# Kernel optimization log

Hardware: AMD Instinct MI355X
Metric: run time of the kernel (lower is better)

Reference implementation:

```python
import jax, jax.numpy as jnp
import numpy as np

NEG_INF = -1.0e12  # matches torch's -1e12 mask value
LEAKY_SLOPE = 0.01  # nn.LeakyReLU default


def setup_inputs() -> dict:
    key = jax.random.key(0)
    k1, k2, k3, k4 = jax.random.split(key, 4)
    B, N, in_c, out_c = 8, 2048, 64, 64
    inp = jax.random.normal(k1, (B, N, in_c), dtype=jnp.float32)
    adj = jax.random.randint(k2, (B, N, N), 0, 2, dtype=jnp.int32)
    W = jax.random.normal(k3, (in_c, out_c), dtype=jnp.float32) * (1.0 / np.sqrt(in_c))
    a = jax.random.normal(k4, (2 * out_c, 1), dtype=jnp.float32) * 0.1
    return {"inp": inp, "adj": adj, "W": W, "a": a}


def reference(inp, adj, W, a):
    # GAT layer. The original builds an O(B*N^2*2*out_c) concat tensor;
    # a^T [h_i || h_j] decomposes exactly into (h_i . a1) + (h_j . a2).
    out_c = W.shape[1]
    h = jnp.einsum('bni,io->bno', inp, W)          # [B,N,out_c]
    a1 = a[:out_c, 0]                               # [out_c]
    a2 = a[out_c:, 0]                               # [out_c]
    e_i = h @ a1                                    # [B,N] source term
    e_j = h @ a2                                    # [B,N] target term
    e = e_i[:, :, None] + e_j[:, None, :]           # [B,N,N]
    e = jnp.where(e > 0, e, LEAKY_SLOPE * e)        # LeakyReLU(0.01)
    masked = jnp.where(adj > 0, e, NEG_INF)
    attention = jax.nn.softmax(masked, axis=2)      # [B,N,N]
    # dropout omitted (eval mode / deterministic reference)
    h_prime = jnp.einsum('bnm,bmo->bno', attention, h)  # [B,N,out_c]
    return h_prime
```

## Files before the change

kernel.cpp:

```cpp
#include <hip/hip_runtime.h>
#include <cstdint>

#define BB 8
#define NN 2048
#define CC 64
#define TI 128
#define JSPLIT 2
#define KRANGE (NN / JSPLIT)
#define JCH 128
#define NCH (KRANGE / JCH)

typedef __attribute__((ext_vector_type(8))) _Float16 f16x8;
typedef __attribute__((ext_vector_type(4))) float f32x4;
typedef __attribute__((ext_vector_type(4))) unsigned int u32x4;
typedef __attribute__((ext_vector_type(4))) int i32x4;

static const size_t WS_H   = 0;
static const size_t WS_E1  = WS_H  + (size_t)BB*NN*CC;
static const size_t WS_E2  = WS_E1 + (size_t)BB*NN;
static const size_t WS_HT  = WS_E2 + (size_t)BB*NN;
static const size_t WS_ACC = WS_HT + (size_t)BB*CC*NN/2;
static const size_t WS_Z   = WS_ACC + (size_t)JSPLIT*BB*NN*CC;

#define GL16(g, l) __builtin_amdgcn_global_load_lds( \
    (const __attribute__((address_space(1))) void*)(g), \
    (__attribute__((address_space(3))) void*)(uint32_t)(uintptr_t)(l), 16, 0, 0)
#define GL4(g, l) __builtin_amdgcn_global_load_lds( \
    (const __attribute__((address_space(1))) void*)(g), \
    (__attribute__((address_space(3))) void*)(uint32_t)(uintptr_t)(l), 4, 0, 0)
#define WAIT0()  asm volatile("s_waitcnt vmcnt(0)" ::: "memory")
#define BAR()    __builtin_amdgcn_s_barrier()

__global__ __launch_bounds__(256) void k1_proj(const float* __restrict__ inp,
        const float* __restrict__ Wm, const float* __restrict__ av,
        float* __restrict__ h, float* __restrict__ e1, float* __restrict__ e2) {
    __shared__ float inp_lds[256];
    int t = threadIdx.x;
    size_t base = (size_t)blockIdx.x * 256;
    inp_lds[t] = inp[base + t];
    __syncthreads();
    int r = t >> 6;
    int c = t & 63;
    const float* irow = &inp_lds[r * 64];
    float acc = 0.f;
    #pragma unroll
    for (int k = 0; k < 64; k++) acc = fmaf(irow[k], Wm[k * 64 + c], acc);
    size_t row = (size_t)blockIdx.x * 4 + r;
    h[row * 64 + c] = acc;
    float v1 = acc * av[c];
    float v2 = acc * av[64 + c];
    #pragma unroll
    for (int o = 32; o > 0; o >>= 1) {
        v1 += __shfl_down(v1, o);
        v2 += __shfl_down(v2, o);
    }
    if (c == 0) { e1[row] = v1; e2[row] = v2; }
}

__global__ __launch_bounds__(256) void k1b_transpose(const float* __restrict__ h,
        unsigned short* __restrict__ hT) {
    __shared__ float tile[64][65];
    int t = threadIdx.x;
    int b = blockIdx.x >> 5;
    int i0 = (blockIdx.x & 31) * 64;
    const float* hb = h + ((size_t)b * NN + i0) * CC;
    #pragma unroll
    for (int q = 0; q < 16; q++) {
        int idx = q * 256 + t;
        tile[idx >> 6][idx & 63] = hb[idx];
    }
    __syncthreads();
    int c = t & 63;
    int rgrp = t >> 6;
    unsigned int uh[8];
    #pragma unroll
    for (int p = 0; p < 8; p++) {
        unsigned int pack_h = 0;
        #pragma unroll
        for (int s = 0; s < 2; s++) {
            float v = tile[rgrp * 16 + p * 2 + s][c];
            _Float16 fh = (_Float16)v;
            unsigned int u = (unsigned int)__builtin_bit_cast(unsigned short, fh);
            pack_h |= u << (16 * s);
        }
        uh[p] = pack_h;
    }
    size_t off = ((size_t)b * 64 + c) * NN + i0 + rgrp * 16;
    u32x4* dh = (u32x4*)(hT + off);
    dh[0] = u32x4{uh[0], uh[1], uh[2], uh[3]};
    dh[1] = u32x4{uh[4], uh[5], uh[6], uh[7]};
}

__global__ __launch_bounds__(512, 1) void k2_mfma(const int* __restrict__ adj,
        const unsigned short* __restrict__ hT,
        const float* __restrict__ e1, const float* __restrict__ e2,
        float* __restrict__ accp, float* __restrict__ zp) {
    __shared__ __align__(16) char smem[135168];
    float* e2L = (float*)(smem + 131072);

    int bid = blockIdx.x;
    int b    = bid & 7;
    int rest = bid >> 3;
    int s    = rest & 1;
    int tile = rest >> 1;
    int i0 = tile * TI;
    int jbase = s * KRANGE;

    int t = threadIdx.x;
    int w = t >> 6;
    int l = t & 63;
    int col = l & 15;
    int kg  = l >> 4;

    const int* adjrow = adj + ((size_t)b * NN + i0 + w * 16 + col) * NN + jbase;
    float e1v = e1[(size_t)b * NN + i0 + w * 16 + col];
    const float* e2b = e2 + (size_t)b * NN;
    const unsigned short* hTb = hT + (size_t)b * 64 * NN;

    f32x4 acc[4];
    #pragma unroll
    for (int n = 0; n < 4; n++) acc[n] = f32x4{0.f, 0.f, 0.f, 0.f};
    f32x4 accZ = f32x4{0.f, 0.f, 0.f, 0.f};

    _Float16 onev = (_Float16)1.0f, zerov = (_Float16)0.0f;
    f16x8 onesf;
    #pragma unroll
    for (int i = 0; i < 8; i++) onesf[i] = (col == 0) ? onev : zerov;

    i32x4 aA[8], aB[8];

#define ADJP(jcN, arr) { \
    _Pragma("unroll") \
    for (int q = 0; q < 4; q++) { \
        const i32x4* ap = (const i32x4*)(adjrow + (jcN) * JCH + q * 32 + kg * 8); \
        arr[2 * q]     = ap[0]; \
        arr[2 * q + 1] = ap[1]; \
    } \
}

#define COMPUTE(jcN, arr) { \
    _Pragma("unroll") \
    for (int ks4 = 0; ks4 < 4; ks4++) { \
        int ks = (jcN) * 4 + ks4; \
        int krel = ks * 32 + kg * 8; \
        i32x4 a0 = arr[2 * ks4]; \
        i32x4 a1 = arr[2 * ks4 + 1]; \
        f32x4 e20 = *(const f32x4*)(e2L + krel); \
        f32x4 e21 = *(const f32x4*)(e2L + krel + 4); \
        float xs[8] = {e20.x, e20.y, e20.z, e20.w, e21.x, e21.y, e21.z, e21.w}; \
        int ms[8] = {a0.x, a0.y, a0.z, a0.w, a1.x, a1.y, a1.z, a1.w}; \
        f16x8 pf; \
        _Pragma("unroll") \
        for (int i = 0; i < 8; i++) { \
            float x = e1v + xs[i]; \
            x = fmaxf(x, 0.01f * x); \
            x = __expf(x); \
            x = (ms[i] > 0) ? x : 0.0f; \
            pf[i] = (_Float16)x; \
        } \
        int g = ks * 4 + kg; \
        _Pragma("unroll") \
        for (int n = 0; n < 4; n++) { \
            int c = n * 16 + col; \
            int p = (g & 120) | ((g ^ c) & 7); \
            f16x8 hv = __builtin_bit_cast(f16x8, *(const f32x4*)(smem + c * 2048 + p * 16)); \
            acc[n] = __builtin_amdgcn_mfma_f32_16x16x32_f16(pf, hv, acc[n], 0, 0, 0); \
        } \
        accZ = __builtin_amdgcn_mfma_f32_16x16x32_f16(pf, onesf, accZ, 0, 0, 0); \
    } \
}

    ADJP(0, aA);

    #pragma unroll
    for (int it = 0; it < 16; it++) {
        int k16 = it * 8 + w;
        int c   = k16 >> 1;
        int p   = (k16 & 1) * 64 + l;
        int g   = (p & 120) | ((p ^ c) & 7);
        const unsigned short* src = hTb + (size_t)c * NN + jbase + g * 8;
        GL16(src, smem + (size_t)k16 * 1024);
    }
    #pragma unroll
    for (int it = 0; it < 2; it++) {
        GL4(e2b + jbase + it * 512 + w * 64 + l,
            smem + 131072 + (it * 512 + w * 64) * 4);
    }
    WAIT0();
    BAR();

    #pragma unroll
    for (int jc = 0; jc < NCH; jc += 2) {
        ADJP(jc + 1, aB);
        COMPUTE(jc, aA);
        if (jc + 2 < NCH) ADJP(jc + 2, aA);
        COMPUTE(jc + 1, aB);
    }

    size_t orow = (size_t)s * BB * NN + (size_t)b * NN + i0 + w * 16 + kg * 4;
    float* accout = accp + orow * CC;
    #pragma unroll
    for (int n = 0; n < 4; n++) {
        #pragma unroll
        for (int r = 0; r < 4; r++) {
            accout[(size_t)r * CC + n * 16 + col] = acc[n][r];
        }
    }
    if (col == 0) {
        #pragma unroll
        for (int r = 0; r < 4; r++) zp[orow + r] = accZ[r];
    }
#undef ADJP
#undef COMPUTE
}

__global__ __launch_bounds__(256) void k3_final(const float* __restrict__ accp,
        const float* __restrict__ zp, float* __restrict__ out) {
    int idx = blockIdx.x * 256 + threadIdx.x;
    const int TOT4 = BB * NN * CC / 4;
    if (idx >= TOT4) return;
    int row = idx >> 4;
    f32x4 s0 = ((const f32x4*)accp)[idx];
    f32x4 s1 = ((const f32x4*)accp)[idx + TOT4];
    float z = zp[row] + zp[row + BB * NN];
    float inv = (z > 0.f) ? (1.0f / z) : 0.f;
    f32x4 o;
    o.x = (s0.x + s1.x) * inv;
    o.y = (s0.y + s1.y) * inv;
    o.z = (s0.z + s1.z) * inv;
    o.w = (s0.w + s1.w) * inv;
    ((f32x4*)out)[idx] = o;
}

extern "C" void kernel_launch(void* const* d_in, const int* in_sizes, int n_in,
                              void* d_out, int out_size, void* d_ws, size_t ws_size,
                              hipStream_t stream) {
    const float* inp = (const float*)d_in[0];
    const int*   adj = (const int*)d_in[1];
    const float* Wm  = (const float*)d_in[2];
    const float* av  = (const float*)d_in[3];
    float* ws = (float*)d_ws;
    float* h    = ws + WS_H;
    float* e1   = ws + WS_E1;
    float* e2   = ws + WS_E2;
    unsigned short* hT = (unsigned short*)(ws + WS_HT);
    float* accp = ws + WS_ACC;
    float* zp   = ws + WS_Z;
    float* out  = (float*)d_out;

    k1_proj<<<BB * NN / 4, 256, 0, stream>>>(inp, Wm, av, h, e1, e2);
    k1b_transpose<<<BB * (NN / 64), 256, 0, stream>>>(h, hT);
    k2_mfma<<<BB * (NN / TI) * JSPLIT, 512, 0, stream>>>(adj, hT, e1, e2, accp, zp);
    k3_final<<<(BB * NN * CC / 4 + 255) / 256, 256, 0, stream>>>(accp, zp, out);
}
```

Before: 44.89 us.

## Fuse projection with fp16 transpose and deepen adjacency prefetch to three buffers

Merges the projection kernel and the transpose kernel into one. Each block now computes a 64-row tile of h in LDS-backed registers and writes e1/e2 plus the transposed fp16 h directly, so the fp32 h round trip and one launch go away. Separately, the main MFMA kernel now uses three adjacency register buffers instead of two, issuing loads two chunks ahead to hide more global-memory latency. The cost is more register pressure in the main kernel and a heavier, lower-parallelism projection kernel.

After: 136.4 us. 3.04x slower.

```diff
diff --git a/kernel.cpp b/kernel.cpp
--- a/kernel.cpp
+++ b/kernel.cpp
@@ -15,8 +15,7 @@
 typedef __attribute__((ext_vector_type(4))) unsigned int u32x4;
 typedef __attribute__((ext_vector_type(4))) int i32x4;
 
-static const size_t WS_H   = 0;
-static const size_t WS_E1  = WS_H  + (size_t)BB*NN*CC;
+static const size_t WS_E1  = 0;
 static const size_t WS_E2  = WS_E1 + (size_t)BB*NN;
 static const size_t WS_HT  = WS_E2 + (size_t)BB*NN;
 static const size_t WS_ACC = WS_HT + (size_t)BB*CC*NN/2;
@@ -31,61 +30,60 @@
 #define WAIT0()  asm volatile("s_waitcnt vmcnt(0)" ::: "memory")
 #define BAR()    __builtin_amdgcn_s_barrier()
 
-__global__ __launch_bounds__(256) void k1_proj(const float* __restrict__ inp,
+__global__ __launch_bounds__(256) void k1_fused(const float* __restrict__ inp,
         const float* __restrict__ Wm, const float* __restrict__ av,
-        float* __restrict__ h, float* __restrict__ e1, float* __restrict__ e2) {
-    __shared__ float inp_lds[256];
-    int t = threadIdx.x;
-    size_t base = (size_t)blockIdx.x * 256;
-    inp_lds[t] = inp[base + t];
-    __syncthreads();
-    int r = t >> 6;
-    int c = t & 63;
-    const float* irow = &inp_lds[r * 64];
-    float acc = 0.f;
-    #pragma unroll
-    for (int k = 0; k < 64; k++) acc = fmaf(irow[k], Wm[k * 64 + c], acc);
-    size_t row = (size_t)blockIdx.x * 4 + r;
-    h[row * 64 + c] = acc;
-    float v1 = acc * av[c];
-    float v2 = acc * av[64 + c];
-    #pragma unroll
-    for (int o = 32; o > 0; o >>= 1) {
-        v1 += __shfl_down(v1, o);
-        v2 += __shfl_down(v2, o);
-    }
-    if (c == 0) { e1[row] = v1; e2[row] = v2; }
-}
-
-__global__ __launch_bounds__(256) void k1b_transpose(const float* __restrict__ h,
-        unsigned short* __restrict__ hT) {
-    __shared__ float tile[64][65];
+        unsigned short* __restrict__ hT, float* __restrict__ e1, float* __restrict__ e2) {
+    __shared__ float inpL[64][65];
+    __shared__ float WL[64][65];
     int t = threadIdx.x;
     int b = blockIdx.x >> 5;
     int i0 = (blockIdx.x & 31) * 64;
-    const float* hb = h + ((size_t)b * NN + i0) * CC;
+    const float* ib = inp + ((size_t)b * NN + i0) * CC;
     #pragma unroll
     for (int q = 0; q < 16; q++) {
         int idx = q * 256 + t;
-        tile[idx >> 6][idx & 63] = hb[idx];
+        inpL[idx >> 6][idx & 63] = ib[idx];
+        WL[idx >> 6][idx & 63]   = Wm[idx];
     }
     __syncthreads();
-    int c = t & 63;
-    int rgrp = t >> 6;
+    int rg = t >> 6;
+    int c  = t & 63;
+    float a1 = av[c], a2 = av[64 + c];
+    float hv[16];
+    #pragma unroll
+    for (int p = 0; p < 16; p++) {
+        float acc = 0.f;
+        #pragma unroll
+        for (int k = 0; k < 64; k++) acc = fmaf(inpL[rg * 16 + p][k], WL[k][c], acc);
+        hv[p] = acc;
+    }
+    #pragma unroll
+    for (int p = 0; p < 16; p++) {
+        float v1 = hv[p] * a1;
+        float v2 = hv[p] * a2;
+        #pragma unroll
+        for (int o = 32; o > 0; o >>= 1) {
+            v1 += __shfl_down(v1, o);
+            v2 += __shfl_down(v2, o);
+        }
+        if (c == 0) {
+            size_t row = (size_t)b * NN + i0 + rg * 16 + p;
+            e1[row] = v1;
+            e2[row] = v2;
+        }
+    }
     unsigned int uh[8];
     #pragma unroll
-    for (int p = 0; p < 8; p++) {
-        unsigned int pack_h = 0;
-        #pragma unroll
-        for (int s = 0; s < 2; s++) {
-            float v = tile[rgrp * 16 + p * 2 + s][c];
-            _Float16 fh = (_Float16)v;
-            unsigned int u = (unsigned int)__builtin_bit_cast(unsigned short, fh);
-            pack_h |= u << (16 * s);
-        }
-        uh[p] = pack_h;
-    }
-    size_t off = ((size_t)b * 64 + c) * NN + i0 + rgrp * 16;
+    for (int p8 = 0; p8 < 8; p8++) {
+        unsigned int pack = 0;
+        #pragma unroll
+        for (int ss = 0; ss < 2; ss++) {
+            _Float16 fh = (_Float16)hv[p8 * 2 + ss];
+            pack |= ((unsigned int)__builtin_bit_cast(unsigned short, fh)) << (16 * ss);
+        }
+        uh[p8] = pack;
+    }
+    size_t off = ((size_t)b * 64 + c) * NN + i0 + rg * 16;
     u32x4* dh = (u32x4*)(hT + off);
     dh[0] = u32x4{uh[0], uh[1], uh[2], uh[3]};
     dh[1] = u32x4{uh[4], uh[5], uh[6], uh[7]};
@@ -127,7 +125,7 @@
     #pragma unroll
     for (int i = 0; i < 8; i++) onesf[i] = (col == 0) ? onev : zerov;
 
-    i32x4 aA[8], aB[8];
+    i32x4 aA[8], aB[8], aC[8];
 
 #define ADJP(jcN, arr) { \
     _Pragma("unroll") \
@@ -171,6 +169,8 @@
 }
 
     ADJP(0, aA);
+    ADJP(1, aB);
+    ADJP(2, aC);
 
     #pragma unroll
     for (int it = 0; it < 16; it++) {
@@ -189,13 +189,14 @@
     WAIT0();
     BAR();
 
-    #pragma unroll
-    for (int jc = 0; jc < NCH; jc += 2) {
-        ADJP(jc + 1, aB);
-        COMPUTE(jc, aA);
-        if (jc + 2 < NCH) ADJP(jc + 2, aA);
-        COMPUTE(jc + 1, aB);
-    }
+    COMPUTE(0, aA); ADJP(3, aA);
+    COMPUTE(1, aB); ADJP(4, aB);
+    COMPUTE(2, aC); ADJP(5, aC);
+    COMPUTE(3, aA); ADJP(6, aA);
+    COMPUTE(4, aB); ADJP(7, aB);
+    COMPUTE(5, aC);
+    COMPUTE(6, aA);
+    COMPUTE(7, aB);
 
     size_t orow = (size_t)s * BB * NN + (size_t)b * NN + i0 + w * 16 + kg * 4;
     float* accout = accp + orow * CC;
@@ -240,7 +241,6 @@
     const float* Wm  = (const float*)d_in[2];
     const float* av  = (const float*)d_in[3];
     float* ws = (float*)d_ws;
-    float* h    = ws + WS_H;
     float* e1   = ws + WS_E1;
     float* e2   = ws + WS_E2;
     unsigned short* hT = (unsigned short*)(ws + WS_HT);
@@ -248,8 +248,7 @@
     float* zp   = ws + WS_Z;
     float* out  = (float*)d_out;
 
-    k1_proj<<<BB * NN / 4, 256, 0, stream>>>(inp, Wm, av, h, e1, e2);
-    k1b_transpose<<<BB * (NN / 64), 256, 0, stream>>>(h, hT);
+    k1_fused<<<BB * (NN / 64), 256, 0, stream>>>(inp, Wm, av, hT, e1, e2);
     k2_mfma<<<BB * (NN / TI) * JSPLIT, 512, 0, stream>>>(adj, hT, e1, e2, accp, zp);
     k3_final<<<(BB * NN * CC / 4 + 255) / 256, 256, 0, stream>>>(accp, zp, out);
 }
```

## Pre-pack adjacency into bitmask in separate kernel before attention MFMA

Applied to the files above, without the earlier changes.

Adds a kernel that reads the int32 adjacency matrix once and packs it into a bit mask laid out to match the MFMA lane layout. The attention kernel then loads a few mask words per lane instead of streaming int32 adjacency inside the compute loop, and the double-buffered prefetch is removed. The full adjacency read still happens, now in a separate pass that cannot overlap with the exp/MFMA work. The transpose kernel's block-to-batch mapping is also changed.

Result: slower. 59.22 us (+31.9%).

```diff
diff --git a/kernel.cpp b/kernel.cpp
--- a/kernel.cpp
+++ b/kernel.cpp
@@ -7,8 +7,7 @@
 #define TI 128
 #define JSPLIT 2
 #define KRANGE (NN / JSPLIT)
-#define JCH 128
-#define NCH (KRANGE / JCH)
+#define NCH 8
 
 typedef __attribute__((ext_vector_type(8))) _Float16 f16x8;
 typedef __attribute__((ext_vector_type(4))) float f32x4;
@@ -21,6 +20,7 @@
 static const size_t WS_HT  = WS_E2 + (size_t)BB*NN;
 static const size_t WS_ACC = WS_HT + (size_t)BB*CC*NN/2;
 static const size_t WS_Z   = WS_ACC + (size_t)JSPLIT*BB*NN*CC;
+static const size_t WS_MSK = WS_Z   + (size_t)JSPLIT*BB*NN;
 
 #define GL16(g, l) __builtin_amdgcn_global_load_lds( \
     (const __attribute__((address_space(1))) void*)(g), \
@@ -30,6 +30,30 @@
     (__attribute__((address_space(3))) void*)(uint32_t)(uintptr_t)(l), 4, 0, 0)
 #define WAIT0()  asm volatile("s_waitcnt vmcnt(0)" ::: "memory")
 #define BAR()    __builtin_amdgcn_s_barrier()
+
+__global__ __launch_bounds__(256) void kpack(const int* __restrict__ adj,
+        unsigned char* __restrict__ mask) {
+    int bid = blockIdx.x;
+    int b = bid & 7;
+    int rowgrp = bid >> 3;
+    int w = threadIdx.x >> 6;
+    int l = threadIdx.x & 63;
+    int row = rowgrp * 4 + w;
+    const int* ar = adj + ((size_t)b * NN + row) * NN + l * 32;
+    i32x4 a[8];
+    #pragma unroll
+    for (int q = 0; q < 8; q++) a[q] = ((const i32x4*)ar)[q];
+    #pragma unroll
+    for (int kg = 0; kg < 4; kg++) {
+        unsigned int byte = 0;
+        #pragma unroll
+        for (int i = 0; i < 4; i++) {
+            byte |= (a[2 * kg][i]     > 0 ? 1u : 0u) << i;
+            byte |= (a[2 * kg + 1][i] > 0 ? 1u : 0u) << (i + 4);
+        }
+        mask[(((size_t)b * 4 + kg) * NN + row) * 64 + l] = (unsigned char)byte;
+    }
+}
 
 __global__ __launch_bounds__(256) void k1_proj(const float* __restrict__ inp,
         const float* __restrict__ Wm, const float* __restrict__ av,
@@ -61,8 +85,8 @@
         unsigned short* __restrict__ hT) {
     __shared__ float tile[64][65];
     int t = threadIdx.x;
-    int b = blockIdx.x >> 5;
-    int i0 = (blockIdx.x & 31) * 64;
+    int b = blockIdx.x & 7;
+    int i0 = ((blockIdx.x >> 3) & 31) * 64;
     const float* hb = h + ((size_t)b * NN + i0) * CC;
     #pragma unroll
     for (int q = 0; q < 16; q++) {
@@ -91,7 +115,7 @@
     dh[1] = u32x4{uh[4], uh[5], uh[6], uh[7]};
 }
 
-__global__ __launch_bounds__(512, 1) void k2_mfma(const int* __restrict__ adj,
+__global__ __launch_bounds__(512, 1) void k2_mfma(const unsigned char* __restrict__ mask,
         const unsigned short* __restrict__ hT,
         const float* __restrict__ e1, const float* __restrict__ e2,
         float* __restrict__ accp, float* __restrict__ zp) {
@@ -112,11 +136,16 @@
     int col = l & 15;
     int kg  = l >> 4;
 
-    const int* adjrow = adj + ((size_t)b * NN + i0 + w * 16 + col) * NN + jbase;
-    float e1v = e1[(size_t)b * NN + i0 + w * 16 + col];
+    int myrow = i0 + w * 16 + col;
+    float e1v = e1[(size_t)b * NN + myrow];
     const float* e2b = e2 + (size_t)b * NN;
     const unsigned short* hTb = hT + (size_t)b * 64 * NN;
 
+    const unsigned char* mrow = mask + (((size_t)b * 4 + kg) * NN + myrow) * 64 + s * 32;
+    u32x4 m0 = *(const u32x4*)(mrow);
+    u32x4 m1 = *(const u32x4*)(mrow + 16);
+    unsigned int mm[8] = {m0.x, m0.y, m0.z, m0.w, m1.x, m1.y, m1.z, m1.w};
+
     f32x4 acc[4];
     #pragma unroll
     for (int n = 0; n < 4; n++) acc[n] = f32x4{0.f, 0.f, 0.f, 0.f};
@@ -127,35 +156,40 @@
     #pragma unroll
     for (int i = 0; i < 8; i++) onesf[i] = (col == 0) ? onev : zerov;
 
-    i32x4 aA[8], aB[8];
-
-#define ADJP(jcN, arr) { \
-    _Pragma("unroll") \
-    for (int q = 0; q < 4; q++) { \
-        const i32x4* ap = (const i32x4*)(adjrow + (jcN) * JCH + q * 32 + kg * 8); \
-        arr[2 * q]     = ap[0]; \
-        arr[2 * q + 1] = ap[1]; \
-    } \
-}
-
-#define COMPUTE(jcN, arr) { \
+    #pragma unroll
+    for (int it = 0; it < 16; it++) {
+        int k16 = it * 8 + w;
+        int c   = k16 >> 1;
+        int p   = (k16 & 1) * 64 + l;
+        int g   = (p & 120) | ((p ^ c) & 7);
+        const unsigned short* src = hTb + (size_t)c * NN + jbase + g * 8;
+        GL16(src, smem + (size_t)k16 * 1024);
+    }
+    #pragma unroll
+    for (int it = 0; it < 2; it++) {
+        GL4(e2b + jbase + it * 512 + w * 64 + l,
+            smem + 131072 + (it * 512 + w * 64) * 4);
+    }
+    WAIT0();
+    BAR();
+
+#define COMPUTE(jcN) { \
+    unsigned int mword = mm[jcN]; \
     _Pragma("unroll") \
     for (int ks4 = 0; ks4 < 4; ks4++) { \
         int ks = (jcN) * 4 + ks4; \
         int krel = ks * 32 + kg * 8; \
-        i32x4 a0 = arr[2 * ks4]; \
-        i32x4 a1 = arr[2 * ks4 + 1]; \
+        unsigned int mbyte = (mword >> (ks4 * 8)) & 0xffu; \
         f32x4 e20 = *(const f32x4*)(e2L + krel); \
         f32x4 e21 = *(const f32x4*)(e2L + krel + 4); \
         float xs[8] = {e20.x, e20.y, e20.z, e20.w, e21.x, e21.y, e21.z, e21.w}; \
-        int ms[8] = {a0.x, a0.y, a0.z, a0.w, a1.x, a1.y, a1.z, a1.w}; \
         f16x8 pf; \
         _Pragma("unroll") \
         for (int i = 0; i < 8; i++) { \
             float x = e1v + xs[i]; \
             x = fmaxf(x, 0.01f * x); \
             x = __expf(x); \
-            x = (ms[i] > 0) ? x : 0.0f; \
+            x = ((mbyte >> i) & 1u) ? x : 0.0f; \
             pf[i] = (_Float16)x; \
         } \
         int g = ks * 4 + kg; \
@@ -170,32 +204,8 @@
     } \
 }
 
-    ADJP(0, aA);
-
-    #pragma unroll
-    for (int it = 0; it < 16; it++) {
-        int k16 = it * 8 + w;
-        int c   = k16 >> 1;
-        int p   = (k16 & 1) * 64 + l;
-        int g   = (p & 120) | ((p ^ c) & 7);
-        const unsigned short* src = hTb + (size_t)c * NN + jbase + g * 8;
-        GL16(src, smem + (size_t)k16 * 1024);
-    }
-    #pragma unroll
-    for (int it = 0; it < 2; it++) {
-        GL4(e2b + jbase + it * 512 + w * 64 + l,
-            smem + 131072 + (it * 512 + w * 64) * 4);
-    }
-    WAIT0();
-    BAR();
-
-    #pragma unroll
-    for (int jc = 0; jc < NCH; jc += 2) {
-        ADJP(jc + 1, aB);
-        COMPUTE(jc, aA);
-        if (jc + 2 < NCH) ADJP(jc + 2, aA);
-        COMPUTE(jc + 1, aB);
-    }
+    #pragma unroll
+    for (int jc = 0; jc < NCH; jc++) COMPUTE(jc);
 
     size_t orow = (size_t)s * BB * NN + (size_t)b * NN + i0 + w * 16 + kg * 4;
     float* accout = accp + orow * CC;
@@ -210,7 +220,6 @@
         #pragma unroll
         for (int r = 0; r < 4; r++) zp[orow + r] = accZ[r];
     }
-#undef ADJP
 #undef COMPUTE
 }
 
@@ -246,10 +255,12 @@
     unsigned short* hT = (unsigned short*)(ws + WS_HT);
     float* accp = ws + WS_ACC;
     float* zp   = ws + WS_Z;
+    unsigned char* mask = (unsigned char*)(ws + WS_MSK);
     float* out  = (float*)d_out;
 
+    kpack<<<BB * (NN / 4), 256, 0, stream>>>(adj, mask);
     k1_proj<<<BB * NN / 4, 256, 0, stream>>>(inp, Wm, av, h, e1, e2);
     k1b_transpose<<<BB * (NN / 64), 256, 0, stream>>>(h, hT);
-    k2_mfma<<<BB * (NN / TI) * JSPLIT, 512, 0, stream>>>(adj, hT, e1, e2, accp, zp);
+    k2_mfma<<<BB * (NN / TI) * JSPLIT, 512, 0, stream>>>(mask, hT, e1, e2, accp, zp);
     k3_final<<<(BB * NN * CC / 4 + 255) / 256, 256, 0, stream>>>(accp, zp, out);
 }
```

## Factor exp of LeakyReLU into precomputed per-node fp16 exponentials

Applied to the files above, without the earlier changes.

Because exp is monotonic, exp(leaky(e1+e2)) equals max(exp(e1)exp(e2), exp(0.01 e1)exp(0.01 e2)). The per-node exponentials are precomputed in fp16 in the projection kernel, so the inner loop does packed fp16 multiplies, a max and a mask multiply instead of one exp per attention entry. The mask is built arithmetically from the int adjacency values. Storing exponentials without max-subtraction risks fp16 overflow or underflow for large logits. The transpose kernel's block-to-batch mapping is also reordered.

Measured after the change: 45.00 us. No clear change (+0.2%).

```diff
diff --git a/kernel.cpp b/kernel.cpp
--- a/kernel.cpp
+++ b/kernel.cpp
@@ -11,14 +11,16 @@
 #define NCH (KRANGE / JCH)
 
 typedef __attribute__((ext_vector_type(8))) _Float16 f16x8;
+typedef __attribute__((ext_vector_type(2))) _Float16 f16x2;
 typedef __attribute__((ext_vector_type(4))) float f32x4;
 typedef __attribute__((ext_vector_type(4))) unsigned int u32x4;
 typedef __attribute__((ext_vector_type(4))) int i32x4;
 
 static const size_t WS_H   = 0;
 static const size_t WS_E1  = WS_H  + (size_t)BB*NN*CC;
-static const size_t WS_E2  = WS_E1 + (size_t)BB*NN;
-static const size_t WS_HT  = WS_E2 + (size_t)BB*NN;
+static const size_t WS_BF  = WS_E1 + (size_t)BB*NN;
+static const size_t WS_bf  = WS_BF + (size_t)BB*NN/2;
+static const size_t WS_HT  = WS_bf + (size_t)BB*NN/2;
 static const size_t WS_ACC = WS_HT + (size_t)BB*CC*NN/2;
 static const size_t WS_Z   = WS_ACC + (size_t)JSPLIT*BB*NN*CC;
 
@@ -33,7 +35,8 @@
 
 __global__ __launch_bounds__(256) void k1_proj(const float* __restrict__ inp,
         const float* __restrict__ Wm, const float* __restrict__ av,
-        float* __restrict__ h, float* __restrict__ e1, float* __restrict__ e2) {
+        float* __restrict__ h, float* __restrict__ e1,
+        unsigned short* __restrict__ Bf, unsigned short* __restrict__ bf) {
     __shared__ float inp_lds[256];
     int t = threadIdx.x;
     size_t base = (size_t)blockIdx.x * 256;
@@ -54,15 +57,19 @@
         v1 += __shfl_down(v1, o);
         v2 += __shfl_down(v2, o);
     }
-    if (c == 0) { e1[row] = v1; e2[row] = v2; }
+    if (c == 0) {
+        e1[row] = v1;
+        Bf[row] = __builtin_bit_cast(unsigned short, (_Float16)__expf(v2));
+        bf[row] = __builtin_bit_cast(unsigned short, (_Float16)__expf(0.01f * v2));
+    }
 }
 
 __global__ __launch_bounds__(256) void k1b_transpose(const float* __restrict__ h,
         unsigned short* __restrict__ hT) {
     __shared__ float tile[64][65];
     int t = threadIdx.x;
-    int b = blockIdx.x >> 5;
-    int i0 = (blockIdx.x & 31) * 64;
+    int b = blockIdx.x & 7;
+    int i0 = ((blockIdx.x >> 3) & 31) * 64;
     const float* hb = h + ((size_t)b * NN + i0) * CC;
     #pragma unroll
     for (int q = 0; q < 16; q++) {
@@ -93,10 +100,12 @@
 
 __global__ __launch_bounds__(512, 1) void k2_mfma(const int* __restrict__ adj,
         const unsigned short* __restrict__ hT,
-        const float* __restrict__ e1, const float* __restrict__ e2,
+        const float* __restrict__ e1, const unsigned short* __restrict__ Bf,
+        const unsigned short* __restrict__ bf,
         float* __restrict__ accp, float* __restrict__ zp) {
     __shared__ __align__(16) char smem[135168];
-    float* e2L = (float*)(smem + 131072);
+    char* BL = smem + 131072;
+    char* bL = smem + 133120;
 
     int bid = blockIdx.x;
     int b    = bid & 7;
@@ -114,7 +123,12 @@
 
     const int* adjrow = adj + ((size_t)b * NN + i0 + w * 16 + col) * NN + jbase;
     float e1v = e1[(size_t)b * NN + i0 + w * 16 + col];
-    const float* e2b = e2 + (size_t)b * NN;
+    _Float16 Ah = (_Float16)__expf(e1v);
+    _Float16 ah = (_Float16)__expf(0.01f * e1v);
+    f16x2 A2 = {Ah, Ah};
+    f16x2 a2 = {ah, ah};
+    const unsigned short* Bfb = Bf + (size_t)b * NN;
+    const unsigned short* bfb = bf + (size_t)b * NN;
     const unsigned short* hTb = hT + (size_t)b * 64 * NN;
 
     f32x4 acc[4];
@@ -142,22 +156,27 @@
     _Pragma("unroll") \
     for (int ks4 = 0; ks4 < 4; ks4++) { \
         int ks = (jcN) * 4 + ks4; \
-        int krel = ks * 32 + kg * 8; \
+        int krel2 = (ks * 32 + kg * 8) * 2; \
         i32x4 a0 = arr[2 * ks4]; \
         i32x4 a1 = arr[2 * ks4 + 1]; \
-        f32x4 e20 = *(const f32x4*)(e2L + krel); \
-        f32x4 e21 = *(const f32x4*)(e2L + krel + 4); \
-        float xs[8] = {e20.x, e20.y, e20.z, e20.w, e21.x, e21.y, e21.z, e21.w}; \
+        u32x4 Bu = __builtin_bit_cast(u32x4, *(const f32x4*)(BL + krel2)); \
+        u32x4 bu = __builtin_bit_cast(u32x4, *(const f32x4*)(bL + krel2)); \
         int ms[8] = {a0.x, a0.y, a0.z, a0.w, a1.x, a1.y, a1.z, a1.w}; \
-        f16x8 pf; \
+        unsigned int Bw[4] = {Bu.x, Bu.y, Bu.z, Bu.w}; \
+        unsigned int bw[4] = {bu.x, bu.y, bu.z, bu.w}; \
+        unsigned int pfu[4]; \
         _Pragma("unroll") \
-        for (int i = 0; i < 8; i++) { \
-            float x = e1v + xs[i]; \
-            x = fmaxf(x, 0.01f * x); \
-            x = __expf(x); \
-            x = (ms[i] > 0) ? x : 0.0f; \
-            pf[i] = (_Float16)x; \
+        for (int i = 0; i < 4; i++) { \
+            f16x2 Bp = __builtin_bit_cast(f16x2, Bw[i]); \
+            f16x2 bp = __builtin_bit_cast(f16x2, bw[i]); \
+            f16x2 hi = A2 * Bp; \
+            f16x2 lo = a2 * bp; \
+            f16x2 mx = __builtin_elementwise_max(hi, lo); \
+            unsigned int fm = ((unsigned int)ms[2 * i] | ((unsigned int)ms[2 * i + 1] << 16)) * 0x3C00u; \
+            f16x2 pm = __builtin_bit_cast(f16x2, fm); \
+            pfu[i] = __builtin_bit_cast(unsigned int, (f16x2)(mx * pm)); \
         } \
+        f16x8 pf = __builtin_bit_cast(f16x8, u32x4{pfu[0], pfu[1], pfu[2], pfu[3]}); \
         int g = ks * 4 + kg; \
         _Pragma("unroll") \
         for (int n = 0; n < 4; n++) { \
@@ -181,11 +200,8 @@
         const unsigned short* src = hTb + (size_t)c * NN + jbase + g * 8;
         GL16(src, smem + (size_t)k16 * 1024);
     }
-    #pragma unroll
-    for (int it = 0; it < 2; it++) {
-        GL4(e2b + jbase + it * 512 + w * 64 + l,
-            smem + 131072 + (it * 512 + w * 64) * 4);
-    }
+    GL4(Bfb + jbase + w * 128 + l * 2, BL + w * 256);
+    GL4(bfb + jbase + w * 128 + l * 2, bL + w * 256);
     WAIT0();
     BAR();
 
@@ -242,14 +258,15 @@
     float* ws = (float*)d_ws;
     float* h    = ws + WS_H;
     float* e1   = ws + WS_E1;
-    float* e2   = ws + WS_E2;
+    unsigned short* Bf = (unsigned short*)(ws + WS_BF);
+    unsigned short* bf = (unsigned short*)(ws + WS_bf);
     unsigned short* hT = (unsigned short*)(ws + WS_HT);
     float* accp = ws + WS_ACC;
     float* zp   = ws + WS_Z;
     float* out  = (float*)d_out;
 
-    k1_proj<<<BB * NN / 4, 256, 0, stream>>>(inp, Wm, av, h, e1, e2);
+    k1_proj<<<BB * NN / 4, 256, 0, stream>>>(inp, Wm, av, h, e1, Bf, bf);
     k1b_transpose<<<BB * (NN / 64), 256, 0, stream>>>(h, hT);
-    k2_mfma<<<BB * (NN / TI) * JSPLIT, 512, 0, stream>>>(adj, hT, e1, e2, accp, zp);
+    k2_mfma<<<BB * (NN / TI) * JSPLIT, 512, 0, stream>>>(adj, hT, e1, Bf, bf, accp, zp);
     k3_final<<<(BB * NN * CC / 4 + 255) / 256, 256, 0, stream>>>(accp, zp, out);
 }
```
